# Performance work log

Measured on AMD Instinct MI355X. Metric: run time of the kernel, lower is better.

Reference implementation:

```python
import jax, jax.numpy as jnp
import numpy as np

ITERATIONS = 20
EPS = 1e-9

def setup_inputs() -> dict:
    key = jax.random.key(0)
    x = jax.random.normal(key, (8192, 64, 64), dtype=jnp.float32)
    return {"x": x}

def reference(x):
    M = jnp.exp(x)
    def body(_, M):
        M = M / (jnp.sum(M, axis=-1, keepdims=True) + EPS)
        M = M / (jnp.sum(M, axis=-2, keepdims=True) + EPS)
        return M
    M = jax.lax.fori_loop(0, ITERATIONS, body, M)
    return M
```

## Files before the change

### kernel.cpp

```cpp
#include <hip/hip_runtime.h>

#define ITERS 20
#define EPS 1e-9f

typedef float v2f __attribute__((ext_vector_type(2)));


template <int CTRL>
__device__ __forceinline__ float dpp_add(float x) {
    int yi = __builtin_amdgcn_update_dpp(0, __float_as_int(x), CTRL, 0xf, 0xf, true);
    return x + __int_as_float(yi);
}

#if __has_builtin(__builtin_amdgcn_permlane16_swap)
__device__ __forceinline__ float xadd16(float x) {
    unsigned u = __float_as_uint(x);
    auto r = __builtin_amdgcn_permlane16_swap(u, u, false, false);
    return __uint_as_float(r[0]) + __uint_as_float(r[1]);
}
#else
__device__ __forceinline__ float xadd16(float x) {
    return x + __int_as_float(__builtin_amdgcn_ds_swizzle(__float_as_int(x), 0x401F));
}
#endif

#if __has_builtin(__builtin_amdgcn_permlane32_swap)
__device__ __forceinline__ float xadd32(float x) {
    unsigned u = __float_as_uint(x);
    auto r = __builtin_amdgcn_permlane32_swap(u, u, false, false);
    return __uint_as_float(r[0]) + __uint_as_float(r[1]);
}
#else
__device__ __forceinline__ float xadd32(float x) {
    return x + __shfl_xor(x, 32, 64);
}
#endif

__global__ __launch_bounds__(256, 4) void sinkhorn_kernel(
        const float* __restrict__ x, float* __restrict__ out, int nmat) {
    const int lane = threadIdx.x & 63;
    const int wave = threadIdx.x >> 6;
    const int mat  = blockIdx.x * 4 + wave;
    if (mat >= nmat) return;
    const int bi = lane >> 3;
    const int bj = lane & 7;

    const float4* __restrict__ xin = (const float4*)(x + (size_t)mat * 4096);

    v2f b2[8][4];
    #pragma unroll
    for (int r = 0; r < 8; ++r) {
        float4 lo = xin[(8 * bi + r) * 16 + 2 * bj + 0];
        float4 hi = xin[(8 * bi + r) * 16 + 2 * bj + 1];
        b2[r][0] = (v2f){__expf(lo.x), __expf(lo.y)};
        b2[r][1] = (v2f){__expf(lo.z), __expf(lo.w)};
        b2[r][2] = (v2f){__expf(hi.x), __expf(hi.y)};
        b2[r][3] = (v2f){__expf(hi.z), __expf(hi.w)};
    }

    float uu[8];
    v2f   vv2[4];
    #pragma unroll
    for (int i = 0; i < 8; ++i) uu[i] = 1.0f;
    #pragma unroll
    for (int i = 0; i < 4; ++i) vv2[i] = (v2f){1.0f, 1.0f};

    for (int it = 0; it < ITERS; ++it) {
        float p[8];
        #pragma unroll
        for (int r = 0; r < 8; ++r) {
            v2f s2 = b2[r][0] * vv2[0];
            s2 += b2[r][1] * vv2[1];
            s2 += b2[r][2] * vv2[2];
            s2 += b2[r][3] * vv2[3];
            p[r] = s2.x + s2.y;
        }
        #pragma unroll
        for (int r = 0; r < 8; ++r) p[r] = dpp_add<0xB1>(p[r]);
        #pragma unroll
        for (int r = 0; r < 8; ++r) p[r] = dpp_add<0x4E>(p[r]);
        #pragma unroll
        for (int r = 0; r < 8; ++r) p[r] = dpp_add<0x141>(p[r]);
        #pragma unroll
        for (int r = 0; r < 8; ++r) {
            float S = fmaf(uu[r], p[r], EPS);
            uu[r] *= __builtin_amdgcn_rcpf(S);
        }

        v2f q2[4];
        #pragma unroll
        for (int c = 0; c < 4; ++c) q2[c] = b2[0][c] * uu[0];
        #pragma unroll
        for (int r = 1; r < 8; ++r) {
            #pragma unroll
            for (int c = 0; c < 4; ++c) q2[c] += b2[r][c] * uu[r];
        }
        #pragma unroll
        for (int c = 0; c < 4; ++c) {
            q2[c].x = dpp_add<0x128>(q2[c].x);
            q2[c].y = dpp_add<0x128>(q2[c].y);
        }
        #pragma unroll
        for (int c = 0; c < 4; ++c) {
            q2[c].x = xadd16(q2[c].x);
            q2[c].y = xadd16(q2[c].y);
        }
        #pragma unroll
        for (int c = 0; c < 4; ++c) {
            q2[c].x = xadd32(q2[c].x);
            q2[c].y = xadd32(q2[c].y);
        }
        #pragma unroll
        for (int c = 0; c < 4; ++c) {
            float Tx = fmaf(vv2[c].x, q2[c].x, EPS);
            float Ty = fmaf(vv2[c].y, q2[c].y, EPS);
            vv2[c].x *= __builtin_amdgcn_rcpf(Tx);
            vv2[c].y *= __builtin_amdgcn_rcpf(Ty);
        }
    }

    float4* __restrict__ o = (float4*)(out + (size_t)mat * 4096);
    #pragma unroll
    for (int r = 0; r < 8; ++r) {
        v2f uv0 = vv2[0] * uu[r];
        v2f uv1 = vv2[1] * uu[r];
        v2f uv2 = vv2[2] * uu[r];
        v2f uv3 = vv2[3] * uu[r];
        v2f w0 = b2[r][0] * uv0;
        v2f w1 = b2[r][1] * uv1;
        v2f w2 = b2[r][2] * uv2;
        v2f w3 = b2[r][3] * uv3;
        float4 lo, hi;
        lo.x = w0.x; lo.y = w0.y; lo.z = w1.x; lo.w = w1.y;
        hi.x = w2.x; hi.y = w2.y; hi.z = w3.x; hi.w = w3.y;
        o[(8 * bi + r) * 16 + 2 * bj + 0] = lo;
        o[(8 * bi + r) * 16 + 2 * bj + 1] = hi;
    }
}

extern "C" void kernel_launch(void* const* d_in, const int* in_sizes, int n_in,
                              void* d_out, int out_size, void* d_ws, size_t ws_size,
                              hipStream_t stream) {
    const float* x = (const float*)d_in[0];
    float* out = (float*)d_out;
    const int nmat = in_sizes[0] / 4096;
    const int blocks = (nmat + 3) / 4;
    sinkhorn_kernel<<<blocks, 256, 0, stream>>>(x, out, nmat);
}
```

Measured before the change: 250.1 us.

## Split each matrix across two waves with LDS row-sum exchange

New measurement: 264.8 us. +5.8%, slower.

```diff
diff --git a/kernel.cpp b/kernel.cpp
--- a/kernel.cpp
+++ b/kernel.cpp
@@ -36,43 +36,44 @@
 }
 #endif
 
-__global__ __launch_bounds__(256, 4) void sinkhorn_kernel(
+__global__ __launch_bounds__(256, 6) void sinkhorn_kernel(
         const float* __restrict__ x, float* __restrict__ out, int nmat) {
-    const int lane = threadIdx.x & 63;
-    const int wave = threadIdx.x >> 6;
-    const int mat  = blockIdx.x * 4 + wave;
-    if (mat >= nmat) return;
+    __shared__ float xch[2][2][2][64];
+
+    const int lane  = threadIdx.x & 63;
+    const int wave  = threadIdx.x >> 6;
+    const int mslot = wave >> 1;
+    const int w     = wave & 1;
+    int mat = blockIdx.x * 2 + mslot;
+    if (mat >= nmat) mat = nmat - 1;
     const int bi = lane >> 3;
     const int bj = lane & 7;
 
     const float4* __restrict__ xin = (const float4*)(x + (size_t)mat * 4096);
 
-    v2f b2[8][4];
+    v2f b2[8][2];
     #pragma unroll
     for (int r = 0; r < 8; ++r) {
-        float4 lo = xin[(8 * bi + r) * 16 + 2 * bj + 0];
-        float4 hi = xin[(8 * bi + r) * 16 + 2 * bj + 1];
-        b2[r][0] = (v2f){__expf(lo.x), __expf(lo.y)};
-        b2[r][1] = (v2f){__expf(lo.z), __expf(lo.w)};
-        b2[r][2] = (v2f){__expf(hi.x), __expf(hi.y)};
-        b2[r][3] = (v2f){__expf(hi.z), __expf(hi.w)};
+        float4 t = xin[(8 * bi + r) * 16 + 8 * w + bj];
+        b2[r][0] = (v2f){__expf(t.x), __expf(t.y)};
+        b2[r][1] = (v2f){__expf(t.z), __expf(t.w)};
     }
 
     float uu[8];
-    v2f   vv2[4];
+    v2f   vv2[2];
     #pragma unroll
     for (int i = 0; i < 8; ++i) uu[i] = 1.0f;
-    #pragma unroll
-    for (int i = 0; i < 4; ++i) vv2[i] = (v2f){1.0f, 1.0f};
+    vv2[0] = (v2f){1.0f, 1.0f};
+    vv2[1] = (v2f){1.0f, 1.0f};
 
     for (int it = 0; it < ITERS; ++it) {
+        const int slot = it & 1;
+
         float p[8];
         #pragma unroll
         for (int r = 0; r < 8; ++r) {
             v2f s2 = b2[r][0] * vv2[0];
             s2 += b2[r][1] * vv2[1];
-            s2 += b2[r][2] * vv2[2];
-            s2 += b2[r][3] * vv2[3];
             p[r] = s2.x + s2.y;
         }
         #pragma unroll
@@ -81,60 +82,60 @@
         for (int r = 0; r < 8; ++r) p[r] = dpp_add<0x4E>(p[r]);
         #pragma unroll
         for (int r = 0; r < 8; ++r) p[r] = dpp_add<0x141>(p[r]);
+
+        if (bj == 0) {
+            #pragma unroll
+            for (int r = 0; r < 8; ++r) xch[slot][mslot][w][bi * 8 + r] = p[r];
+        }
+        __syncthreads();
+        #pragma unroll
+        for (int r = 0; r < 8; ++r) p[r] += xch[slot][mslot][1 - w][bi * 8 + r];
+
         #pragma unroll
         for (int r = 0; r < 8; ++r) {
             float S = fmaf(uu[r], p[r], EPS);
             uu[r] *= __builtin_amdgcn_rcpf(S);
         }
 
-        v2f q2[4];
+        v2f qe0 = b2[0][0] * uu[0];
+        v2f qe1 = b2[0][1] * uu[0];
+        v2f qo0 = b2[1][0] * uu[1];
+        v2f qo1 = b2[1][1] * uu[1];
         #pragma unroll
-        for (int c = 0; c < 4; ++c) q2[c] = b2[0][c] * uu[0];
-        #pragma unroll
-        for (int r = 1; r < 8; ++r) {
-            #pragma unroll
-            for (int c = 0; c < 4; ++c) q2[c] += b2[r][c] * uu[r];
+        for (int r = 2; r < 8; r += 2) {
+            qe0 += b2[r][0] * uu[r];
+            qe1 += b2[r][1] * uu[r];
+            qo0 += b2[r + 1][0] * uu[r + 1];
+            qo1 += b2[r + 1][1] * uu[r + 1];
         }
-        #pragma unroll
-        for (int c = 0; c < 4; ++c) {
-            q2[c].x = dpp_add<0x128>(q2[c].x);
-            q2[c].y = dpp_add<0x128>(q2[c].y);
-        }
-        #pragma unroll
-        for (int c = 0; c < 4; ++c) {
-            q2[c].x = xadd16(q2[c].x);
-            q2[c].y = xadd16(q2[c].y);
-        }
-        #pragma unroll
-        for (int c = 0; c < 4; ++c) {
-            q2[c].x = xadd32(q2[c].x);
-            q2[c].y = xadd32(q2[c].y);
-        }
-        #pragma unroll
-        for (int c = 0; c < 4; ++c) {
-            float Tx = fmaf(vv2[c].x, q2[c].x, EPS);
-            float Ty = fmaf(vv2[c].y, q2[c].y, EPS);
-            vv2[c].x *= __builtin_amdgcn_rcpf(Tx);
-            vv2[c].y *= __builtin_amdgcn_rcpf(Ty);
-        }
+        v2f q0 = qe0 + qo0;
+        v2f q1 = qe1 + qo1;
+
+        float qa = dpp_add<0x128>(q0.x);
+        float qb = dpp_add<0x128>(q0.y);
+        float qc = dpp_add<0x128>(q1.x);
+        float qd = dpp_add<0x128>(q1.y);
+        qa = xadd16(qa); qb = xadd16(qb); qc = xadd16(qc); qd = xadd16(qd);
+        qa = xadd32(qa); qb = xadd32(qb); qc = xadd32(qc); qd = xadd32(qd);
+
+        float Ta = fmaf(vv2[0].x, qa, EPS);
+        float Tb = fmaf(vv2[0].y, qb, EPS);
+        float Tc = fmaf(vv2[1].x, qc, EPS);
+        float Td = fmaf(vv2[1].y, qd, EPS);
+        vv2[0].x *= __builtin_amdgcn_rcpf(Ta);
+        vv2[0].y *= __builtin_amdgcn_rcpf(Tb);
+        vv2[1].x *= __builtin_amdgcn_rcpf(Tc);
+        vv2[1].y *= __builtin_amdgcn_rcpf(Td);
     }
 
     float4* __restrict__ o = (float4*)(out + (size_t)mat * 4096);
     #pragma unroll
     for (int r = 0; r < 8; ++r) {
-        v2f uv0 = vv2[0] * uu[r];
-        v2f uv1 = vv2[1] * uu[r];
-        v2f uv2 = vv2[2] * uu[r];
-        v2f uv3 = vv2[3] * uu[r];
-        v2f w0 = b2[r][0] * uv0;
-        v2f w1 = b2[r][1] * uv1;
-        v2f w2 = b2[r][2] * uv2;
-        v2f w3 = b2[r][3] * uv3;
-        float4 lo, hi;
-        lo.x = w0.x; lo.y = w0.y; lo.z = w1.x; lo.w = w1.y;
-        hi.x = w2.x; hi.y = w2.y; hi.z = w3.x; hi.w = w3.y;
-        o[(8 * bi + r) * 16 + 2 * bj + 0] = lo;
-        o[(8 * bi + r) * 16 + 2 * bj + 1] = hi;
+        v2f w0 = b2[r][0] * (vv2[0] * uu[r]);
+        v2f w1 = b2[r][1] * (vv2[1] * uu[r]);
+        float4 t;
+        t.x = w0.x; t.y = w0.y; t.z = w1.x; t.w = w1.y;
+        o[(8 * bi + r) * 16 + 8 * w + bj] = t;
     }
 }
 
@@ -144,6 +145,6 @@
     const float* x = (const float*)d_in[0];
     float* out = (float*)d_out;
     const int nmat = in_sizes[0] / 4096;
-    const int blocks = (nmat + 3) / 4;
+    const int blocks = (nmat + 1) / 2;
     sinkhorn_kernel<<<blocks, 256, 0, stream>>>(x, out, nmat);
 }
```

## Process two matrices per wave and drop EPS with direct reciprocal scaling

Applied to the files above, without the earlier changes.

After: 271.7 us. 1.09x slower.

```diff
diff --git a/kernel.cpp b/kernel.cpp
--- a/kernel.cpp
+++ b/kernel.cpp
@@ -1,9 +1,6 @@
 #include <hip/hip_runtime.h>
 
 #define ITERS 20
-#define EPS 1e-9f
-
-typedef float v2f __attribute__((ext_vector_type(2)));
 
 
 template <int CTRL>
@@ -36,105 +33,121 @@
 }
 #endif
 
-__global__ __launch_bounds__(256, 4) void sinkhorn_kernel(
+__global__ __launch_bounds__(256, 2) void sinkhorn_kernel(
         const float* __restrict__ x, float* __restrict__ out, int nmat) {
     const int lane = threadIdx.x & 63;
     const int wave = threadIdx.x >> 6;
-    const int mat  = blockIdx.x * 4 + wave;
-    if (mat >= nmat) return;
+    const int wid  = blockIdx.x * 4 + wave;
+    const int matA = wid * 2;
+    if (matA >= nmat) return;
+    const int matB = matA + 1;
+    const bool hasB = (matB < nmat);
     const int bi = lane >> 3;
     const int bj = lane & 7;
 
-    const float4* __restrict__ xin = (const float4*)(x + (size_t)mat * 4096);
+    const float4* __restrict__ xa = (const float4*)(x + (size_t)matA * 4096);
+    const float4* __restrict__ xb = (const float4*)(x + (size_t)(hasB ? matB : matA) * 4096);
 
-    v2f b2[8][4];
+    float A[8][8], B[8][8];
     #pragma unroll
     for (int r = 0; r < 8; ++r) {
-        float4 lo = xin[(8 * bi + r) * 16 + 2 * bj + 0];
-        float4 hi = xin[(8 * bi + r) * 16 + 2 * bj + 1];
-        b2[r][0] = (v2f){__expf(lo.x), __expf(lo.y)};
-        b2[r][1] = (v2f){__expf(lo.z), __expf(lo.w)};
-        b2[r][2] = (v2f){__expf(hi.x), __expf(hi.y)};
-        b2[r][3] = (v2f){__expf(hi.z), __expf(hi.w)};
+        float4 alo = xa[(8 * bi + r) * 16 + 2 * bj + 0];
+        float4 ahi = xa[(8 * bi + r) * 16 + 2 * bj + 1];
+        float4 blo = xb[(8 * bi + r) * 16 + 2 * bj + 0];
+        float4 bhi = xb[(8 * bi + r) * 16 + 2 * bj + 1];
+        A[r][0] = __expf(alo.x); A[r][1] = __expf(alo.y);
+        A[r][2] = __expf(alo.z); A[r][3] = __expf(alo.w);
+        A[r][4] = __expf(ahi.x); A[r][5] = __expf(ahi.y);
+        A[r][6] = __expf(ahi.z); A[r][7] = __expf(ahi.w);
+        B[r][0] = __expf(blo.x); B[r][1] = __expf(blo.y);
+        B[r][2] = __expf(blo.z); B[r][3] = __expf(blo.w);
+        B[r][4] = __expf(bhi.x); B[r][5] = __expf(bhi.y);
+        B[r][6] = __expf(bhi.z); B[r][7] = __expf(bhi.w);
     }
 
-    float uu[8];
-    v2f   vv2[4];
+    float ua[8], va[8], ub[8], vb[8];
     #pragma unroll
-    for (int i = 0; i < 8; ++i) uu[i] = 1.0f;
-    #pragma unroll
-    for (int i = 0; i < 4; ++i) vv2[i] = (v2f){1.0f, 1.0f};
+    for (int i = 0; i < 8; ++i) { ua[i] = 1.0f; va[i] = 1.0f; ub[i] = 1.0f; vb[i] = 1.0f; }
 
     for (int it = 0; it < ITERS; ++it) {
-        float p[8];
+        float pa[8], pb[8];
         #pragma unroll
         for (int r = 0; r < 8; ++r) {
-            v2f s2 = b2[r][0] * vv2[0];
-            s2 += b2[r][1] * vv2[1];
-            s2 += b2[r][2] * vv2[2];
-            s2 += b2[r][3] * vv2[3];
-            p[r] = s2.x + s2.y;
+            float sae = A[r][0] * va[0], sao = A[r][1] * va[1];
+            float sbe = B[r][0] * vb[0], sbo = B[r][1] * vb[1];
+            sae = fmaf(A[r][2], va[2], sae); sbe = fmaf(B[r][2], vb[2], sbe);
+            sao = fmaf(A[r][3], va[3], sao); sbo = fmaf(B[r][3], vb[3], sbo);
+            sae = fmaf(A[r][4], va[4], sae); sbe = fmaf(B[r][4], vb[4], sbe);
+            sao = fmaf(A[r][5], va[5], sao); sbo = fmaf(B[r][5], vb[5], sbo);
+            sae = fmaf(A[r][6], va[6], sae); sbe = fmaf(B[r][6], vb[6], sbe);
+            sao = fmaf(A[r][7], va[7], sao); sbo = fmaf(B[r][7], vb[7], sbo);
+            pa[r] = sae + sao;
+            pb[r] = sbe + sbo;
         }
         #pragma unroll
-        for (int r = 0; r < 8; ++r) p[r] = dpp_add<0xB1>(p[r]);
+        for (int r = 0; r < 8; ++r) { pa[r] = dpp_add<0xB1>(pa[r]);  pb[r] = dpp_add<0xB1>(pb[r]); }
         #pragma unroll
-        for (int r = 0; r < 8; ++r) p[r] = dpp_add<0x4E>(p[r]);
+        for (int r = 0; r < 8; ++r) { pa[r] = dpp_add<0x4E>(pa[r]);  pb[r] = dpp_add<0x4E>(pb[r]); }
         #pragma unroll
-        for (int r = 0; r < 8; ++r) p[r] = dpp_add<0x141>(p[r]);
+        for (int r = 0; r < 8; ++r) { pa[r] = dpp_add<0x141>(pa[r]); pb[r] = dpp_add<0x141>(pb[r]); }
         #pragma unroll
         for (int r = 0; r < 8; ++r) {
-            float S = fmaf(uu[r], p[r], EPS);
-            uu[r] *= __builtin_amdgcn_rcpf(S);
+            ua[r] = __builtin_amdgcn_rcpf(pa[r]);
+            ub[r] = __builtin_amdgcn_rcpf(pb[r]);
         }
 
-        v2f q2[4];
+        float qa[8], qb[8];
         #pragma unroll
-        for (int c = 0; c < 4; ++c) q2[c] = b2[0][c] * uu[0];
-        #pragma unroll
-        for (int r = 1; r < 8; ++r) {
-            #pragma unroll
-            for (int c = 0; c < 4; ++c) q2[c] += b2[r][c] * uu[r];
+        for (int c = 0; c < 8; ++c) {
+            float sae = A[0][c] * ua[0], sao = A[1][c] * ua[1];
+            float sbe = B[0][c] * ub[0], sbo = B[1][c] * ub[1];
+            sae = fmaf(A[2][c], ua[2], sae); sbe = fmaf(B[2][c], ub[2], sbe);
+            sao = fmaf(A[3][c], ua[3], sao); sbo = fmaf(B[3][c], ub[3], sbo);
+            sae = fmaf(A[4][c], ua[4], sae); sbe = fmaf(B[4][c], ub[4], sbe);
+            sao = fmaf(A[5][c], ua[5], sao); sbo = fmaf(B[5][c], ub[5], sbo);
+            sae = fmaf(A[6][c], ua[6], sae); sbe = fmaf(B[6][c], ub[6], sbe);
+            sao = fmaf(A[7][c], ua[7], sao); sbo = fmaf(B[7][c], ub[7], sbo);
+            qa[c] = sae + sao;
+            qb[c] = sbe + sbo;
         }
         #pragma unroll
-        for (int c = 0; c < 4; ++c) {
-            q2[c].x = dpp_add<0x128>(q2[c].x);
-            q2[c].y = dpp_add<0x128>(q2[c].y);
-        }
+        for (int c = 0; c < 8; ++c) { qa[c] = dpp_add<0x128>(qa[c]); qb[c] = dpp_add<0x128>(qb[c]); }
         #pragma unroll
-        for (int c = 0; c < 4; ++c) {
-            q2[c].x = xadd16(q2[c].x);
-            q2[c].y = xadd16(q2[c].y);
-        }
+        for (int c = 0; c < 8; ++c) { qa[c] = xadd16(qa[c]);         qb[c] = xadd16(qb[c]); }
         #pragma unroll
-        for (int c = 0; c < 4; ++c) {
-            q2[c].x = xadd32(q2[c].x);
-            q2[c].y = xadd32(q2[c].y);
-        }
+        for (int c = 0; c < 8; ++c) { qa[c] = xadd32(qa[c]);         qb[c] = xadd32(qb[c]); }
         #pragma unroll
-        for (int c = 0; c < 4; ++c) {
-            float Tx = fmaf(vv2[c].x, q2[c].x, EPS);
-            float Ty = fmaf(vv2[c].y, q2[c].y, EPS);
-            vv2[c].x *= __builtin_amdgcn_rcpf(Tx);
-            vv2[c].y *= __builtin_amdgcn_rcpf(Ty);
+        for (int c = 0; c < 8; ++c) {
+            va[c] = __builtin_amdgcn_rcpf(qa[c]);
+            vb[c] = __builtin_amdgcn_rcpf(qb[c]);
         }
     }
 
-    float4* __restrict__ o = (float4*)(out + (size_t)mat * 4096);
+    float4* __restrict__ oa = (float4*)(out + (size_t)matA * 4096);
     #pragma unroll
     for (int r = 0; r < 8; ++r) {
-        v2f uv0 = vv2[0] * uu[r];
-        v2f uv1 = vv2[1] * uu[r];
-        v2f uv2 = vv2[2] * uu[r];
-        v2f uv3 = vv2[3] * uu[r];
-        v2f w0 = b2[r][0] * uv0;
-        v2f w1 = b2[r][1] * uv1;
-        v2f w2 = b2[r][2] * uv2;
-        v2f w3 = b2[r][3] * uv3;
+        float ur = ua[r];
         float4 lo, hi;
-        lo.x = w0.x; lo.y = w0.y; lo.z = w1.x; lo.w = w1.y;
-        hi.x = w2.x; hi.y = w2.y; hi.z = w3.x; hi.w = w3.y;
-        o[(8 * bi + r) * 16 + 2 * bj + 0] = lo;
-        o[(8 * bi + r) * 16 + 2 * bj + 1] = hi;
+        lo.x = A[r][0] * ur * va[0]; lo.y = A[r][1] * ur * va[1];
+        lo.z = A[r][2] * ur * va[2]; lo.w = A[r][3] * ur * va[3];
+        hi.x = A[r][4] * ur * va[4]; hi.y = A[r][5] * ur * va[5];
+        hi.z = A[r][6] * ur * va[6]; hi.w = A[r][7] * ur * va[7];
+        oa[(8 * bi + r) * 16 + 2 * bj + 0] = lo;
+        oa[(8 * bi + r) * 16 + 2 * bj + 1] = hi;
+    }
+    if (hasB) {
+        float4* __restrict__ ob = (float4*)(out + (size_t)matB * 4096);
+        #pragma unroll
+        for (int r = 0; r < 8; ++r) {
+            float ur = ub[r];
+            float4 lo, hi;
+            lo.x = B[r][0] * ur * vb[0]; lo.y = B[r][1] * ur * vb[1];
+            lo.z = B[r][2] * ur * vb[2]; lo.w = B[r][3] * ur * vb[3];
+            hi.x = B[r][4] * ur * vb[4]; hi.y = B[r][5] * ur * vb[5];
+            hi.z = B[r][6] * ur * vb[6]; hi.w = B[r][7] * ur * vb[7];
+            ob[(8 * bi + r) * 16 + 2 * bj + 0] = lo;
+            ob[(8 * bi + r) * 16 + 2 * bj + 1] = hi;
+        }
     }
 }
 
@@ -144,6 +157,7 @@
     const float* x = (const float*)d_in[0];
     float* out = (float*)d_out;
     const int nmat = in_sizes[0] / 4096;
-    const int blocks = (nmat + 3) / 4;
+    const int waves = (nmat + 1) / 2;
+    const int blocks = (waves + 3) / 4;
     sinkhorn_kernel<<<blocks, 256, 0, stream>>>(x, out, nmat);
 }
```
